# Kernel optimization log

Measured on AMD Instinct MI355X. Metric: run time of the kernel, lower is better.

The kernel has to match this reference:

```python
import jax, jax.numpy as jnp
import numpy as np
import math

B, S, D, H = 2, 2048, 4096, 32
HD = D // H  # 128


def setup_inputs() -> dict:
    key = jax.random.key(0)
    ks = jax.random.split(key, 8)
    x = jax.random.normal(ks[0], (B, S, D), dtype=jnp.float32)
    wq = jax.random.normal(ks[1], (D, D), dtype=jnp.float32) * 0.02
    wk = jax.random.normal(ks[2], (D, D), dtype=jnp.float32) * 0.02
    wv = jax.random.normal(ks[3], (D, D), dtype=jnp.float32) * 0.02
    wo = jax.random.normal(ks[4], (D, D), dtype=jnp.float32) * 0.02
    # RoPE frequencies as in LLaMA: theta = 10000^{-2i/hd}
    inv_freq = 1.0 / (10000.0 ** (np.arange(0, HD, 2, dtype=np.float32) / HD))  # [HD/2]
    t = np.arange(S, dtype=np.float32)
    freqs = np.outer(t, inv_freq)  # [S, HD/2]
    freqs_cos = jnp.asarray(np.cos(freqs))
    freqs_sin = jnp.asarray(np.sin(freqs))
    # additive causal mask [1,1,S,S]
    neg = jnp.full((S, S), -1e9, dtype=jnp.float32)
    mask = jnp.triu(neg, k=1)[None, None, :, :]
    return {"x": x, "wq": wq, "wk": wk, "wv": wv, "wo": wo,
            "freqs_cos": freqs_cos, "freqs_sin": freqs_sin, "mask": mask}


def _apply_rope(t, cos, sin):
    # t: [b, s, h, hd]; cos/sin: [s, hd/2]. Complex mult on (even, odd) pairs.
    tr = t.reshape(*t.shape[:-1], HD // 2, 2)
    xr, xi = tr[..., 0], tr[..., 1]
    c = cos[None, :, None, :]
    s = sin[None, :, None, :]
    out_r = xr * c - xi * s
    out_i = xr * s + xi * c
    return jnp.stack([out_r, out_i], axis=-1).reshape(t.shape)


def reference(x, wq, wk, wv, wo, freqs_cos, freqs_sin, mask):
    b, s, d = x.shape
    # projections (nn.Linear: y = x @ W^T)
    xq = (x @ wq.T).reshape(b, s, H, HD)
    xk = (x @ wk.T).reshape(b, s, H, HD)
    xv = (x @ wv.T).reshape(b, s, H, HD)
    xq = _apply_rope(xq, freqs_cos, freqs_sin)
    xk = _apply_rope(xk, freqs_cos, freqs_sin)
    # [b,h,q,k] scores, softmax in fp32, then attend
    scores = jnp.einsum('bqhd,bkhd->bhqk', xq, xk) / math.sqrt(HD)
    scores = scores + mask
    probs = jax.nn.softmax(scores.astype(jnp.float32), axis=-1).astype(xq.dtype)
    out = jnp.einsum('bhqk,bkhd->bqhd', probs, xv).reshape(b, s, d)
    return out @ wo.T
```

## Files before the change

### kernel.cpp

```cpp
#include <hip/hip_runtime.h>

typedef __bf16 bf16x8 __attribute__((ext_vector_type(8)));
typedef float f32x4 __attribute__((ext_vector_type(4)));
typedef float f32x16 __attribute__((ext_vector_type(16)));
typedef unsigned short u16;
typedef unsigned int u32;
typedef u16 u16x8 __attribute__((ext_vector_type(8)));
typedef u16 u16x4 __attribute__((ext_vector_type(4)));
typedef u32 u32x4 __attribute__((ext_vector_type(4)));

#define B_ 2
#define S_ 2048
#define D_ 4096
#define H_ 32
#define HD_ 128
#define SM_SCALE 0.08838834764831845f
#define C2_ 0.12751743f

__device__ __forceinline__ u16 f2bf(float f) {
  __bf16 h = (__bf16)f;
  return __builtin_bit_cast(unsigned short, h);
}
__device__ __forceinline__ float bf2f(u16 u) {
  return (float)__builtin_bit_cast(__bf16, u);
}

#define GLD_TO_LDS16(gsrc, ldst)                                                     \
  __builtin_amdgcn_global_load_lds((__attribute__((address_space(1))) void*)(gsrc),  \
                                   (__attribute__((address_space(3))) void*)(ldst),  \
                                   16, 0, 0)

__global__ __launch_bounds__(256) void cvt5_kernel(const float* __restrict__ s0,
                                                   const float* __restrict__ s1,
                                                   const float* __restrict__ s2,
                                                   const float* __restrict__ s3,
                                                   const float* __restrict__ s4,
                                                   u16* __restrict__ d0,
                                                   u16* __restrict__ d1,
                                                   u16* __restrict__ d2,
                                                   u16* __restrict__ d3,
                                                   u16* __restrict__ d4,
                                                   int n4) {
  const int region = blockIdx.x >> 9;
  const float* src = region == 0 ? s0 : region == 1 ? s1 : region == 2 ? s2
                   : region == 3 ? s3 : s4;
  u16* dst = region == 0 ? d0 : region == 1 ? d1 : region == 2 ? d2
           : region == 3 ? d3 : d4;
  int i = (blockIdx.x & 511) * 256 + threadIdx.x;
  const int stride = 512 * 256;
  for (; i < n4; i += stride) {
    float4 v = reinterpret_cast<const float4*>(src)[i];
    u16x4 o;
    o[0] = f2bf(v.x); o[1] = f2bf(v.y); o[2] = f2bf(v.z); o[3] = f2bf(v.w);
    reinterpret_cast<u16x4*>(dst)[i] = o;
  }
}


#define LGKM0()                                            \
  do {                                                     \
    asm volatile("s_waitcnt lgkmcnt(0)" ::: "memory");     \
    __builtin_amdgcn_sched_barrier(0);                     \
  } while (0)

__device__ __forceinline__ void fill_af(bf16x8 (&dst)[4], const u16* half_base,
                                        int wr, int lane, int ks) {
#pragma unroll
  for (int m = 0; m < 4; ++m) {
    int rr = wr * 64 + m * 16 + (lane & 15);
    int c8 = (ks * 4 + (lane >> 4)) ^ (rr & 7);
    dst[m] = *reinterpret_cast<const bf16x8*>(half_base + rr * 64 + c8 * 8);
  }
}
__device__ __forceinline__ void fill_bf(bf16x8 (&dst)[2][2], const u16* half_base,
                                        int wn, int lane) {
#pragma unroll
  for (int ks = 0; ks < 2; ++ks)
#pragma unroll
    for (int n = 0; n < 2; ++n) {
      int rr = wn * 32 + n * 16 + (lane & 15);
      int c8 = (ks * 4 + (lane >> 4)) ^ (rr & 7);
      dst[ks][n] = *reinterpret_cast<const bf16x8*>(half_base + rr * 64 + c8 * 8);
    }
}

#define MFMA8(MQ, NQ, KS, AF, BF)                                                \
  do {                                                                           \
    __builtin_amdgcn_s_setprio(1);                                               \
    _Pragma("unroll") for (int m = 0; m < 4; ++m)                                \
      _Pragma("unroll") for (int n = 0; n < 2; ++n)                              \
        acc[(MQ) * 4 + m][(NQ) * 2 + n] =                                        \
            __builtin_amdgcn_mfma_f32_16x16x32_bf16(                             \
                (AF)[m], (BF)[KS][n], acc[(MQ) * 4 + m][(NQ) * 2 + n], 0, 0, 0); \
    __builtin_amdgcn_s_setprio(0);                                               \
  } while (0)

template <typename OutT, bool ROPE>
__global__ __launch_bounds__(512, 2) void gemm256_kernel(const u16* __restrict__ A,
                                                         const u16* __restrict__ Bw,
                                                         OutT* __restrict__ C,
                                                         int M, int N, int K,
                                                         const float* __restrict__ fc,
                                                         const float* __restrict__ fs) {
  __shared__ u16 As[2][2][8192];
  __shared__ u16 Bs[2][2][8192];
  const int tid = threadIdx.x;
  const int lane = tid & 63;
  const int w = tid >> 6;
  const int wr = w >> 2;
  const int wn = w & 3;
  const int nbx = N >> 8;
  const int nby = M >> 8;
  const int nwg = nby * nbx;
  int tr, tc;
  if (nby == 16 && nbx == 16) {
    int xcd = blockIdx.x & 7, j = blockIdx.x >> 3;
    tr = (xcd >> 1) * 4 + (j >> 3);
    tc = (xcd & 1) * 8 + (j & 7);
  } else {
    int wg = blockIdx.x;
    if ((nwg & 7) == 0) wg = (wg & 7) * (nwg >> 3) + (wg >> 3);
    tr = wg / nbx; tc = wg % nbx;
  }

  const size_t arow0 = (size_t)tr * 256;
  const size_t brow0 = (size_t)tc * 256;
  const int KT = K >> 6;

  auto stageA = [&](int t, int half) {
    if (t >= KT) return;
    const int k0 = t << 6;
    u16* base = &As[t & 1][half][0];
#pragma unroll
    for (int i = 0; i < 2; ++i) {
      int q = i * 512 + tid;
      int r = q >> 3;
      int c8 = (q & 7) ^ (r & 7);
      GLD_TO_LDS16(A + (arow0 + half * 128 + r) * K + k0 + c8 * 8, base + q * 8);
    }
  };
  auto stageB = [&](int t, int half) {
    if (t >= KT) return;
    const int k0 = t << 6;
    u16* base = &Bs[t & 1][half][0];
#pragma unroll
    for (int i = 0; i < 2; ++i) {
      int q = i * 512 + tid;
      int r = q >> 3;
      int c8 = (q & 7) ^ (r & 7);
      GLD_TO_LDS16(Bw + (brow0 + half * 128 + r) * K + k0 + c8 * 8, base + q * 8);
    }
  };

  f32x4 acc[8][4] = {};
  bf16x8 afX[4], afY[4], bf0[2][2], bf1[2][2];

  stageA(0, 0); stageA(0, 1); stageB(0, 0); stageB(0, 1);
  stageB(1, 0); stageB(1, 1); stageA(1, 1);
  asm volatile("s_waitcnt vmcnt(4)" ::: "memory");
  __builtin_amdgcn_s_barrier();
  __builtin_amdgcn_sched_barrier(0);
  fill_af(afX, &As[0][0][0], wr, lane, 0);
  fill_bf(bf0, &Bs[0][0][0], wn, lane);

  for (int k = 0; k < KT; ++k) {
    const int buf = k & 1, nb = buf ^ 1;
    const u16* A0 = &As[buf][0][0];
    const u16* A1 = &As[buf][1][0];
    const u16* B1L = &Bs[buf][1][0];
    const u16* A0n = &As[nb][0][0];
    const u16* B0n = &Bs[nb][0][0];

    LGKM0();
    fill_af(afY, A0, wr, lane, 1);
    fill_bf(bf1, B1L, wn, lane);
    stageA(k + 1, 0);
    MFMA8(0, 0, 0, afX, bf0);
    LGKM0();
    fill_af(afX, A1, wr, lane, 0);
    MFMA8(0, 0, 1, afY, bf0);
    __builtin_amdgcn_s_barrier();

    LGKM0();
    fill_af(afY, A1, wr, lane, 1);
    stageB(k + 2, 0);
    MFMA8(1, 0, 0, afX, bf0);
    LGKM0();
    fill_af(afX, A1, wr, lane, 0);
    MFMA8(1, 0, 1, afY, bf0);
    __builtin_amdgcn_s_barrier();

    LGKM0();
    fill_af(afY, A1, wr, lane, 1);
    stageB(k + 2, 1);
    MFMA8(1, 1, 0, afX, bf1);
    LGKM0();
    fill_af(afX, A0, wr, lane, 0);
    MFMA8(1, 1, 1, afY, bf1);
    __builtin_amdgcn_s_barrier();

    LGKM0();
    fill_af(afY, A0, wr, lane, 1);
    MFMA8(0, 1, 0, afX, bf1);
    LGKM0();
    stageA(k + 2, 1);
    if (k >= KT - 3) asm volatile("s_waitcnt vmcnt(0)" ::: "memory");
    else             asm volatile("s_waitcnt vmcnt(4)" ::: "memory");
    __builtin_amdgcn_s_barrier();
    __builtin_amdgcn_sched_barrier(0);
    if (k + 1 < KT) {
      fill_af(afX, A0n, wr, lane, 0);
      fill_bf(bf0, B0n, wn, lane);
    }
    MFMA8(0, 1, 1, afY, bf1);
    __builtin_amdgcn_s_barrier();
  }

#pragma unroll
  for (int mi = 0; mi < 8; ++mi) {
    const int mq = mi >> 2, m = mi & 3;
#pragma unroll
    for (int ni = 0; ni < 4; ++ni) {
      const int nq = ni >> 1, n = ni & 1;
#pragma unroll
      for (int r = 0; r < 4; ++r) {
        size_t row = arow0 + mq * 128 + wr * 64 + m * 16 + ((lane >> 4) << 2) + r;
        size_t col = (size_t)tc * 256 + nq * 128 + wn * 32 + n * 16 + (lane & 15);
        float v = acc[mi][ni][r];
        if constexpr (ROPE) {
          float o = __shfl_xor(v, 1);
          int s = (int)(row & (S_ - 1));
          int p = (wn * 32 + n * 16 + (lane & 14)) >> 1;
          float cv = fc[(s << 6) + p];
          float sv = fs[(s << 6) + p];
          v = (lane & 1) ? (v * cv + o * sv) : (v * cv - o * sv);
        }
        if constexpr (__is_same(OutT, float)) {
          C[row * N + col] = v;
        } else {
          C[row * N + col] = f2bf(v);
        }
      }
    }
  }
}

__global__ __launch_bounds__(256, 2) void attn_kernel(const u16* __restrict__ Q,
                                                      const u16* __restrict__ K,
                                                      const u16* __restrict__ V,
                                                      u16* __restrict__ O) {
  __shared__ u16 Ks[2][64 * 128];
  __shared__ u16 Vt[2][128 * 64];

  const int blk = blockIdx.x;
  const int qt = 15 - (blk >> 6);
  const int bh = blk & 63;
  const int b = bh >> 5, h = bh & 31;
  const int q0 = qt << 7;
  const int tid = threadIdx.x, lane = tid & 63, w = tid >> 6;
  const int wq0 = q0 + w * 32;
  const int l31 = lane & 31;
  const int hi = lane >> 5;
  const int qg = wq0 + l31;

  bf16x8 qf[8];
#pragma unroll
  for (int kb = 0; kb < 8; ++kb)
    qf[kb] = *reinterpret_cast<const bf16x8*>(Q + (size_t)(b * S_ + qg) * D_ + h * HD_ + kb * 16 + hi * 8);

  f32x16 oacc[4] = {};
  float mrun = -__builtin_inff(), lrun = 0.f;

  const int ntiles = 2 * qt + 2;
  u16x8 vreg[4];

  {
#pragma unroll
    for (int it = 0; it < 4; ++it) {
      int ff = it * 256 + tid;
      int row = ff >> 4, cc = ff & 15;
      int scc = cc ^ (row & 7);
      GLD_TO_LDS16(K + (size_t)(b * S_ + row) * D_ + h * HD_ + scc * 8, &Ks[0][ff << 3]);
    }
#pragma unroll
    for (int it = 0; it < 4; ++it) {
      int ff = it * 256 + tid;
      int r = ff & 63, dc = ff >> 6;
      vreg[it] = *reinterpret_cast<const u16x8*>(V + (size_t)(b * S_ + r) * D_ + h * HD_ + dc * 8);
    }
#pragma unroll
    for (int it = 0; it < 4; ++it) {
      int ff = it * 256 + tid;
      int r = ff & 63, dc = ff >> 6;
#pragma unroll
      for (int j = 0; j < 8; ++j) {
        int d = dc * 8 + j;
        Vt[0][(d << 6) + (((r >> 3) ^ (d & 7)) << 3) + (r & 7)] = vreg[it][j];
      }
    }
  }
  __syncthreads();

  for (int t = 0; t < ntiles; ++t) {
    const int cur = t & 1, nxt = cur ^ 1;
    const bool pre = (t + 1 < ntiles);
    if (pre) {
      const int kv1 = (t + 1) << 6;
#pragma unroll
      for (int it = 0; it < 4; ++it) {
        int ff = it * 256 + tid;
        int row = ff >> 4, cc = ff & 15;
        int scc = cc ^ (row & 7);
        GLD_TO_LDS16(K + (size_t)(b * S_ + kv1 + row) * D_ + h * HD_ + scc * 8, &Ks[nxt][ff << 3]);
      }
#pragma unroll
      for (int it = 0; it < 4; ++it) {
        int ff = it * 256 + tid;
        int r = ff & 63, dc = ff >> 6;
        vreg[it] = *reinterpret_cast<const u16x8*>(V + (size_t)(b * S_ + kv1 + r) * D_ + h * HD_ + dc * 8);
      }
    }

    const int kv0 = t << 6;
    if (kv0 <= wq0 + 31) {
      f32x16 st[2] = {};
      __builtin_amdgcn_s_setprio(1);
#pragma unroll
      for (int kvh = 0; kvh < 2; ++kvh) {
#pragma unroll
        for (int kb = 0; kb < 8; ++kb) {
          int row = kvh * 32 + l31;
          int cc = (2 * kb + hi) ^ (row & 7);
          bf16x8 kf = *reinterpret_cast<const bf16x8*>(&Ks[cur][(row << 7) + (cc << 3)]);
          st[kvh] = __builtin_amdgcn_mfma_f32_32x32x16_bf16(kf, qf[kb], st[kvh], 0, 0, 0);
        }
      }
      __builtin_amdgcn_s_setprio(0);

      if (kv0 + 63 > wq0) {
#pragma unroll
        for (int kvh = 0; kvh < 2; ++kvh)
#pragma unroll
          for (int r = 0; r < 16; ++r) {
            int kvg = kv0 + kvh * 32 + (r & 3) + 8 * (r >> 2) + 4 * hi;
            if (kvg > qg) st[kvh][r] = -1e30f;
          }
      }

      float vmax = -1e30f;
#pragma unroll
      for (int kvh = 0; kvh < 2; ++kvh)
#pragma unroll
        for (int r = 0; r < 16; ++r) vmax = fmaxf(vmax, st[kvh][r]);
      vmax = fmaxf(vmax, __shfl_xor(vmax, 32));
      if (!__all(vmax <= mrun + 64.0f)) {
        float mnew = fmaxf(mrun, vmax);
        float sc = exp2f((mrun - mnew) * C2_);
        mrun = mnew;
        lrun *= sc;
#pragma unroll
        for (int db = 0; db < 4; ++db)
#pragma unroll
          for (int r = 0; r < 16; ++r) oacc[db][r] *= sc;
      }
      float psum = 0.f;
#pragma unroll
      for (int kvh = 0; kvh < 2; ++kvh)
#pragma unroll
        for (int r = 0; r < 16; ++r) {
          float p = exp2f((st[kvh][r] - mrun) * C2_);
          st[kvh][r] = p;
          psum += p;
        }
      psum += __shfl_xor(psum, 32);
      lrun += psum;

      __builtin_amdgcn_s_setprio(1);
#pragma unroll
      for (int h2 = 0; h2 < 2; ++h2)
#pragma unroll
        for (int s2 = 0; s2 < 2; ++s2) {
          const int rb = s2 * 8;
          u32 w0, w1, w2, w3;
          asm("v_cvt_pk_bf16_f32 %0, %1, %2" : "=v"(w0) : "v"(st[h2][rb + 0]), "v"(st[h2][rb + 1]));
          asm("v_cvt_pk_bf16_f32 %0, %1, %2" : "=v"(w1) : "v"(st[h2][rb + 2]), "v"(st[h2][rb + 3]));
          asm("v_cvt_pk_bf16_f32 %0, %1, %2" : "=v"(w2) : "v"(st[h2][rb + 4]), "v"(st[h2][rb + 5]));
          asm("v_cvt_pk_bf16_f32 %0, %1, %2" : "=v"(w3) : "v"(st[h2][rb + 6]), "v"(st[h2][rb + 7]));
          u32 sw0 = (u32)__shfl_xor((int)w0, 32);
          u32 sw1 = (u32)__shfl_xor((int)w1, 32);
          u32 sw2 = (u32)__shfl_xor((int)w2, 32);
          u32 sw3 = (u32)__shfl_xor((int)w3, 32);
          u32x4 fw;
          fw[0] = hi ? sw2 : w0;
          fw[1] = hi ? sw3 : w1;
          fw[2] = hi ? w2 : sw0;
          fw[3] = hi ? w3 : sw1;
          bf16x8 pfrag = __builtin_bit_cast(bf16x8, fw);
#pragma unroll
          for (int db = 0; db < 4; ++db) {
            int d = db * 32 + l31;
            int cc = (h2 * 4 + s2 * 2 + hi) ^ (d & 7);
            bf16x8 va = *reinterpret_cast<const bf16x8*>(&Vt[cur][(d << 6) + (cc << 3)]);
            oacc[db] = __builtin_amdgcn_mfma_f32_32x32x16_bf16(va, pfrag, oacc[db], 0, 0, 0);
          }
        }
      __builtin_amdgcn_s_setprio(0);
    }

    if (pre) {
#pragma unroll
      for (int it = 0; it < 4; ++it) {
        int ff = it * 256 + tid;
        int r = ff & 63, dc = ff >> 6;
#pragma unroll
        for (int j = 0; j < 8; ++j) {
          int d = dc * 8 + j;
          Vt[nxt][(d << 6) + (((r >> 3) ^ (d & 7)) << 3) + (r & 7)] = vreg[it][j];
        }
      }
    }
    __syncthreads();
  }

  const float rinv = 1.0f / lrun;
#pragma unroll
  for (int db = 0; db < 4; ++db)
#pragma unroll
    for (int g = 0; g < 4; ++g) {
      u16x4 o4;
#pragma unroll
      for (int j = 0; j < 4; ++j) o4[j] = f2bf(oacc[db][g * 4 + j] * rinv);
      int d = db * 32 + g * 8 + 4 * hi;
      *reinterpret_cast<u16x4*>(O + (size_t)(b * S_ + qg) * D_ + h * HD_ + d) = o4;
    }
}

extern "C" void kernel_launch(void* const* d_in, const int* in_sizes, int n_in,
                              void* d_out, int out_size, void* d_ws, size_t ws_size,
                              hipStream_t stream) {
  const float* x = (const float*)d_in[0];
  const float* wq = (const float*)d_in[1];
  const float* wk = (const float*)d_in[2];
  const float* wv = (const float*)d_in[3];
  const float* wo = (const float*)d_in[4];
  const float* fc = (const float*)d_in[5];
  const float* fs = (const float*)d_in[6];
  float* out = (float*)d_out;

  const size_t SLOT = (size_t)B_ * S_ * D_;
  u16* ws = (u16*)d_ws;
  u16* wqb = ws + 0 * SLOT;
  u16* wkb = ws + 1 * SLOT;
  u16* wvb = ws + 2 * SLOT;
  u16* wob = ws + 3 * SLOT;
  u16* xb  = ws + 4 * SLOT;
  u16* Qb  = ws + 5 * SLOT;
  u16* Kb  = ws + 6 * SLOT;
  u16* Vb  = ws + 7 * SLOT;
  u16* Ob  = xb;

  const int n4 = (int)(SLOT / 4);
  cvt5_kernel<<<2560, 256, 0, stream>>>(x, wq, wk, wv, wo, xb, wqb, wkb, wvb, wob, n4);

  gemm256_kernel<u16, true><<<256, 512, 0, stream>>>(xb, wqb, Qb, B_ * S_, D_, D_, fc, fs);
  gemm256_kernel<u16, true><<<256, 512, 0, stream>>>(xb, wkb, Kb, B_ * S_, D_, D_, fc, fs);
  gemm256_kernel<u16, false><<<256, 512, 0, stream>>>(xb, wvb, Vb, B_ * S_, D_, D_, fc, fs);

  attn_kernel<<<1024, 256, 0, stream>>>(Qb, Kb, Vb, Ob);

  gemm256_kernel<float, false><<<256, 512, 0, stream>>>(Ob, wob, out, B_ * S_, D_, D_, fc, fs);
}
```

Measured before the change: 680.4 us.

## Use 256-query attention tiles with 8 waves and packed V transpose stores

The attention kernel now runs 512 threads per block, each block covering 256 query rows, so every K/V tile loaded into LDS is shared by eight waves instead of four and global K/V traffic is halved. The V transpose into LDS is rewritten so each thread loads two adjacent rows and writes packed 32-bit pairs, cutting the number of LDS store instructions. The cost is fewer blocks (512), coarser causal load balance across tiles, and higher per-CU resource pressure from the 512-thread blocks under launch bounds of 2.

```diff
diff --git a/kernel.cpp b/kernel.cpp
--- a/kernel.cpp
+++ b/kernel.cpp
@@ -245,7 +245,7 @@
   }
 }
 
-__global__ __launch_bounds__(256, 2) void attn_kernel(const u16* __restrict__ Q,
+__global__ __launch_bounds__(512, 2) void attn_kernel(const u16* __restrict__ Q,
                                                       const u16* __restrict__ K,
                                                       const u16* __restrict__ V,
                                                       u16* __restrict__ O) {
@@ -253,16 +253,20 @@
   __shared__ u16 Vt[2][128 * 64];
 
   const int blk = blockIdx.x;
-  const int qt = 15 - (blk >> 6);
+  const int qt = 7 - (blk >> 6);
   const int bh = blk & 63;
   const int b = bh >> 5, h = bh & 31;
-  const int q0 = qt << 7;
+  const int q0 = qt << 8;
   const int tid = threadIdx.x, lane = tid & 63, w = tid >> 6;
   const int wq0 = q0 + w * 32;
   const int l31 = lane & 31;
   const int hi = lane >> 5;
   const int qg = wq0 + l31;
 
+  const int r0 = lane >> 1;
+  const int dc = 2 * w + (lane & 1);
+  const int vd0 = dc * 8;
+
   bf16x8 qf[8];
 #pragma unroll
   for (int kb = 0; kb < 8; ++kb)
@@ -271,32 +275,25 @@
   f32x16 oacc[4] = {};
   float mrun = -__builtin_inff(), lrun = 0.f;
 
-  const int ntiles = 2 * qt + 2;
-  u16x8 vreg[4];
+  const int ntiles = 4 * qt + 4;
+  u16x8 vr0, vr1;
 
   {
 #pragma unroll
-    for (int it = 0; it < 4; ++it) {
-      int ff = it * 256 + tid;
+    for (int it = 0; it < 2; ++it) {
+      int ff = it * 512 + tid;
       int row = ff >> 4, cc = ff & 15;
       int scc = cc ^ (row & 7);
       GLD_TO_LDS16(K + (size_t)(b * S_ + row) * D_ + h * HD_ + scc * 8, &Ks[0][ff << 3]);
     }
-#pragma unroll
-    for (int it = 0; it < 4; ++it) {
-      int ff = it * 256 + tid;
-      int r = ff & 63, dc = ff >> 6;
-      vreg[it] = *reinterpret_cast<const u16x8*>(V + (size_t)(b * S_ + r) * D_ + h * HD_ + dc * 8);
-    }
-#pragma unroll
-    for (int it = 0; it < 4; ++it) {
-      int ff = it * 256 + tid;
-      int r = ff & 63, dc = ff >> 6;
-#pragma unroll
-      for (int j = 0; j < 8; ++j) {
-        int d = dc * 8 + j;
-        Vt[0][(d << 6) + (((r >> 3) ^ (d & 7)) << 3) + (r & 7)] = vreg[it][j];
-      }
+    vr0 = *reinterpret_cast<const u16x8*>(V + (size_t)(b * S_ + 2 * r0) * D_ + h * HD_ + vd0);
+    vr1 = *reinterpret_cast<const u16x8*>(V + (size_t)(b * S_ + 2 * r0 + 1) * D_ + h * HD_ + vd0);
+    u32* vt32 = reinterpret_cast<u32*>(&Vt[0][0]);
+#pragma unroll
+    for (int j = 0; j < 8; ++j) {
+      int d = vd0 + j;
+      u32 val = (u32)vr0[j] | ((u32)vr1[j] << 16);
+      vt32[d * 32 + ((r0 >> 2) ^ j) * 4 + (r0 & 3)] = val;
     }
   }
   __syncthreads();
@@ -307,18 +304,14 @@
     if (pre) {
       const int kv1 = (t + 1) << 6;
 #pragma unroll
-      for (int it = 0; it < 4; ++it) {
-        int ff = it * 256 + tid;
+      for (int it = 0; it < 2; ++it) {
+        int ff = it * 512 + tid;
         int row = ff >> 4, cc = ff & 15;
         int scc = cc ^ (row & 7);
         GLD_TO_LDS16(K + (size_t)(b * S_ + kv1 + row) * D_ + h * HD_ + scc * 8, &Ks[nxt][ff << 3]);
       }
-#pragma unroll
-      for (int it = 0; it < 4; ++it) {
-        int ff = it * 256 + tid;
-        int r = ff & 63, dc = ff >> 6;
-        vreg[it] = *reinterpret_cast<const u16x8*>(V + (size_t)(b * S_ + kv1 + r) * D_ + h * HD_ + dc * 8);
-      }
+      vr0 = *reinterpret_cast<const u16x8*>(V + (size_t)(b * S_ + kv1 + 2 * r0) * D_ + h * HD_ + vd0);
+      vr1 = *reinterpret_cast<const u16x8*>(V + (size_t)(b * S_ + kv1 + 2 * r0 + 1) * D_ + h * HD_ + vd0);
     }
 
     const int kv0 = t << 6;
@@ -408,15 +401,12 @@
     }
 
     if (pre) {
-#pragma unroll
-      for (int it = 0; it < 4; ++it) {
-        int ff = it * 256 + tid;
-        int r = ff & 63, dc = ff >> 6;
-#pragma unroll
-        for (int j = 0; j < 8; ++j) {
-          int d = dc * 8 + j;
-          Vt[nxt][(d << 6) + (((r >> 3) ^ (d & 7)) << 3) + (r & 7)] = vreg[it][j];
-        }
+      u32* vt32 = reinterpret_cast<u32*>(&Vt[nxt][0]);
+#pragma unroll
+      for (int j = 0; j < 8; ++j) {
+        int d = vd0 + j;
+        u32 val = (u32)vr0[j] | ((u32)vr1[j] << 16);
+        vt32[d * 32 + ((r0 >> 2) ^ j) * 4 + (r0 & 3)] = val;
       }
     }
     __syncthreads();
@@ -466,7 +456,7 @@
   gemm256_kernel<u16, true><<<256, 512, 0, stream>>>(xb, wkb, Kb, B_ * S_, D_, D_, fc, fs);
   gemm256_kernel<u16, false><<<256, 512, 0, stream>>>(xb, wvb, Vb, B_ * S_, D_, D_, fc, fs);
 
-  attn_kernel<<<1024, 256, 0, stream>>>(Qb, Kb, Vb, Ob);
+  attn_kernel<<<512, 512, 0, stream>>>(Qb, Kb, Vb, Ob);
 
   gemm256_kernel<float, false><<<256, 512, 0, stream>>>(Ob, wob, out, B_ * S_, D_, D_, fc, fs);
 }
```

Measured after the change: 680.2 us. About the same (-0.0%).
